# Kernel tuning notes

Hardware: AMD Instinct MI355X
Metric: run time of the kernel (lower is better)

Reference implementation:

```python
import jax, jax.numpy as jnp
from jax import lax
import numpy as np

L, B, C, H, W = 2, 4, 256, 128, 128
D = C // 2            # complex feature dim per head (embed_dim // 2)
NH = 2                # hardcoded n_heads in ComplexTransformerEncoderLayer
KS, STRIDE, PAD = 9, 8, 4
SCALE = 32.0 ** -0.5  # n_head_channels ** -0.5 (hardcoded 32)

_PNAMES = ['wq','bq','wk','bk','wv','bv','off_dw_w','off_dw_b','off_ln_g','off_ln_b',
           'off_pw_w','fc1_wr','fc1_wi','fc1_br','fc1_bi','fc2_wr','fc2_wi','fc2_br',
           'fc2_bi','ln_grr','ln_gri','ln_gii','ln_br','ln_bi','rpe_table']


def _bilinear(img, grid):
    # img: (Cc, Hi, Wi); grid: (..., 2) with (x, y) in [-1, 1]
    # matches F.grid_sample(mode='bilinear', align_corners=True, padding_mode='zeros')
    Cc, Hi, Wi = img.shape
    x = (grid[..., 0] + 1.0) * 0.5 * (Wi - 1)
    y = (grid[..., 1] + 1.0) * 0.5 * (Hi - 1)
    x0 = jnp.floor(x); y0 = jnp.floor(y)
    x1 = x0 + 1.0; y1 = y0 + 1.0
    wx1 = x - x0; wx0 = 1.0 - wx1
    wy1 = y - y0; wy0 = 1.0 - wy1

    def tap(yy, xx, wgt):
        valid = (xx >= 0) & (xx <= Wi - 1) & (yy >= 0) & (yy <= Hi - 1)
        xi = jnp.clip(xx, 0, Wi - 1).astype(jnp.int32)
        yi = jnp.clip(yy, 0, Hi - 1).astype(jnp.int32)
        v = img[:, yi, xi]                      # (Cc, *grid_shape)
        return v * (wgt * valid.astype(img.dtype))[None]

    return (tap(y0, x0, wy0 * wx0) + tap(y0, x1, wy0 * wx1)
            + tap(y1, x0, wy1 * wx0) + tap(y1, x1, wy1 * wx1))

_grid_sample = jax.vmap(_bilinear)


def _cln(a, b, gam, eps=1e-20):
    # complex layer-norm via 2x2 covariance whitening over the last (feature) dim
    grr, gri, gii, br, bi = gam
    a = a - a.mean(-1, keepdims=True)
    b = b - b.mean(-1, keepdims=True)
    vrr = (a * a).mean(-1, keepdims=True) + eps
    vii = (b * b).mean(-1, keepdims=True) + eps
    vri = (a * b).mean(-1, keepdims=True)
    s = jnp.sqrt(vrr * vii - vri * vri)
    t = jnp.sqrt(vrr + vii + 2.0 * s)
    inv = 1.0 / (s * t)
    wrr = (vii + s) * inv; wii = (vrr + s) * inv; wri = -vri * inv
    na = wrr * a + wri * b
    nb = wri * a + wii * b
    return grr * na + gri * nb + br, gri * na + gii * nb + bi


def _layer(xa, xb, p):
    res_a = xa.reshape(B * NH, D, H * W).transpose(2, 0, 1)  # (HW, B*NH, D)
    res_b = xb.reshape(B * NH, D, H * W).transpose(2, 0, 1)

    def proj(x, w, bias):  # 1x1 conv
        return jnp.einsum('bchw,oc->bohw', x, w) + bias[None, :, None, None]

    qa = proj(xa, p['wq'], p['bq'])
    qb = proj(xb, p['wq'], p['bq'])

    def conv_offset(q):
        y = lax.conv_general_dilated(q, p['off_dw_w'], (STRIDE, STRIDE),
                                     ((PAD, PAD), (PAD, PAD)),
                                     feature_group_count=C,
                                     dimension_numbers=('NCHW', 'OIHW', 'NCHW'))
        y = y + p['off_dw_b'][None, :, None, None]
        m = y.mean(1, keepdims=True)
        v = ((y - m) ** 2).mean(1, keepdims=True)
        y = (y - m) * lax.rsqrt(v + 1e-5)
        y = y * p['off_ln_g'][None, :, None, None] + p['off_ln_b'][None, :, None, None]
        y = jax.nn.gelu(y, approximate=False)
        return jnp.einsum('bchw,pc->bhwp', y, p['off_pw_w'])  # (B, Hk, Wk, 2) in (y, x)

    off_a = conv_offset(qa)
    off_b = conv_offset(qb)
    Hk, Wk = off_a.shape[1], off_a.shape[2]
    ns = Hk * Wk

    ry = jnp.linspace(0.5, Hk - 0.5, Hk) / (Hk - 1.0) * 2.0 - 1.0
    rx = jnp.linspace(0.5, Wk - 0.5, Wk) / (Wk - 1.0) * 2.0 - 1.0
    ref = jnp.stack(jnp.meshgrid(ry, rx, indexing='ij'), -1)  # (Hk, Wk, 2) (y, x)
    pos_a = off_a + ref
    pos_b = off_b + ref

    xs_a = _grid_sample(xa, pos_a[..., ::-1])  # (B, C, Hk, Wk)
    xs_b = _grid_sample(xb, pos_b[..., ::-1])

    ka = proj(xs_a, p['wk'], p['bk']).reshape(B * NH, D, ns)
    va = proj(xs_a, p['wv'], p['bv']).reshape(B * NH, D, ns)
    kb = proj(xs_b, p['wk'], p['bk']).reshape(B * NH, D, ns)
    vb = proj(xs_b, p['wv'], p['bv']).reshape(B * NH, D, ns)
    qa_ = qa.reshape(B * NH, D, H * W)
    qb_ = qb.reshape(B * NH, D, H * W)

    # Re( q * conj(k) ); imaginary part is discarded by attn.real in the original
    attn = SCALE * (jnp.einsum('bcm,bcn->bmn', qa_, ka)
                    + jnp.einsum('bcm,bcn->bmn', qb_, kb))

    # deformable RPE bias; only the real (a) branch survives attn.real
    gy = jnp.arange(H, dtype=xa.dtype) / (H - 1.0) * 2.0 - 1.0
    gx = jnp.arange(W, dtype=xa.dtype) / (W - 1.0) * 2.0 - 1.0
    qg = jnp.stack(jnp.meshgrid(gy, gx, indexing='ij'), -1).reshape(H * W, 2)
    disp_a = (qg[None, :, None, :] - pos_a.reshape(B, ns, 2)[:, None, :, :]) * 0.5
    rpe = jnp.broadcast_to(p['rpe_table'][None], (B, NH, 2 * H - 1, 2 * W - 1))
    bias_a = _grid_sample(rpe, disp_a[..., ::-1]).reshape(B * NH, H * W, ns)

    attn = jax.nn.softmax(attn + bias_a, axis=2)
    oa = jnp.einsum('bmn,bcn->bcm', attn, va).transpose(2, 0, 1)  # (HW, B*NH, D)
    ob = jnp.einsum('bmn,bcn->bcm', attn, vb).transpose(2, 0, 1)

    oa, ob = _cln(oa, ob, (p['ln_grr'][0], p['ln_gri'][0], p['ln_gii'][0],
                           p['ln_br'][0], p['ln_bi'][0]))
    xa2 = res_a + oa
    xb2 = res_b + ob

    def clinear(a, b, wr, wi, br, bi):
        ya = a @ wr.T - b @ wi.T + br
        yb = a @ wi.T + b @ wr.T + bi
        return ya, yb

    ha, hb = clinear(xa2, xb2, p['fc1_wr'], p['fc1_wi'], p['fc1_br'], p['fc1_bi'])
    ha = jax.nn.relu(ha); hb = jax.nn.relu(hb)
    ha, hb = clinear(ha, hb, p['fc2_wr'], p['fc2_wi'], p['fc2_br'], p['fc2_bi'])
    ha, hb = _cln(ha, hb, (p['ln_grr'][1], p['ln_gri'][1], p['ln_gii'][1],
                           p['ln_br'][1], p['ln_bi'][1]))
    xa3 = xa2 + ha
    xb3 = xb2 + hb
    return (xa3.transpose(1, 2, 0).reshape(B, C, H, W),
            xb3.transpose(1, 2, 0).reshape(B, C, H, W))


def _forward(x_A, x_B, stacked):
    for l in range(L):
        p = {n: stacked[n][l] for n in _PNAMES}
        x_A, x_B = _layer(x_A, x_B, p)
    return x_A, x_B


def setup_inputs():
    key = jax.random.key(0)
    ks = jax.random.split(key, 12)
    f32 = jnp.float32
    return {
        'x_A': jax.random.normal(ks[0], (B, C, H, W), f32),
        'x_B': jax.random.normal(ks[1], (B, C, H, W), f32),
        'wq': jax.random.normal(ks[2], (L, C, C), f32) / np.float32(np.sqrt(C)),
        'bq': jnp.zeros((L, C), f32),
        'wk': jax.random.normal(ks[3], (L, C, C), f32) / np.float32(np.sqrt(C)),
        'bk': jnp.zeros((L, C), f32),
        'wv': jax.random.normal(ks[4], (L, C, C), f32) / np.float32(np.sqrt(C)),
        'bv': jnp.zeros((L, C), f32),
        'off_dw_w': jax.random.normal(ks[5], (L, C, 1, KS, KS), f32) * 0.05,
        'off_dw_b': jnp.zeros((L, C), f32),
        'off_ln_g': jnp.ones((L, C), f32),
        'off_ln_b': jnp.zeros((L, C), f32),
        'off_pw_w': jax.random.normal(ks[6], (L, 2, C), f32) * 0.01,
        'fc1_wr': jax.random.normal(ks[7], (L, D, D), f32) / np.float32(np.sqrt(D)),
        'fc1_wi': jax.random.normal(ks[8], (L, D, D), f32) / np.float32(np.sqrt(D)),
        'fc1_br': jnp.zeros((L, D), f32),
        'fc1_bi': jnp.zeros((L, D), f32),
        'fc2_wr': jax.random.normal(ks[9], (L, D, D), f32) / np.float32(np.sqrt(D)),
        'fc2_wi': jax.random.normal(ks[10], (L, D, D), f32) / np.float32(np.sqrt(D)),
        'fc2_br': jnp.zeros((L, D), f32),
        'fc2_bi': jnp.zeros((L, D), f32),
        'ln_grr': jnp.full((L, 2, D), 1.0 / np.sqrt(2.0), f32),
        'ln_gri': jnp.zeros((L, 2, D), f32),
        'ln_gii': jnp.full((L, 2, D), 1.0 / np.sqrt(2.0), f32),
        'ln_br': jnp.zeros((L, 2, D), f32),
        'ln_bi': jnp.zeros((L, 2, D), f32),
        # original forward creates rpe_table as fresh zeros each call
        'rpe_table': jnp.zeros((L, NH, 2 * H - 1, 2 * W - 1), f32),
    }


def reference(x_A, x_B, wq, bq, wk, bk, wv, bv, off_dw_w, off_dw_b, off_ln_g, off_ln_b,
              off_pw_w, fc1_wr, fc1_wi, fc1_br, fc1_bi, fc2_wr, fc2_wi, fc2_br, fc2_bi,
              ln_grr, ln_gri, ln_gii, ln_br, ln_bi, rpe_table):
    vals = (wq, bq, wk, bk, wv, bv, off_dw_w, off_dw_b, off_ln_g, off_ln_b, off_pw_w,
            fc1_wr, fc1_wi, fc1_br, fc1_bi, fc2_wr, fc2_wi, fc2_br, fc2_bi,
            ln_grr, ln_gri, ln_gii, ln_br, ln_bi, rpe_table)
    stacked = {n: v for n, v in zip(_PNAMES, vals)}
    return _forward(x_A, x_B, stacked)
```

## Files before the change

### kernel.cpp

```cpp
#include <hip/hip_runtime.h>
#include <math.h>

#define DEVFN static __device__ __forceinline__

constexpr int LAYERS = 2;
constexpr int Bz = 4;
constexpr int Cc = 256;
constexpr int Hh = 128;
constexpr int Ww = 128;
constexpr int Dd = 128;
constexpr int NHh = 2;
constexpr int BHt = Bz * NHh;
constexpr int Mt  = Hh * Ww;
constexpr int HK = 16, WK = 16;
constexpr int NSs = HK * WK;
constexpr int STR = 8, PADc = 4;
constexpr int RPH = 2*Hh - 1, RPW = 2*Ww - 1;
constexpr float SCALE_F = 0.17677669529663687f;

typedef __attribute__((ext_vector_type(8))) short  bf16x8;
typedef __attribute__((ext_vector_type(4))) float  f32x4;

DEVFN float wsum64(float v) {
    #pragma unroll
    for (int off = 32; off > 0; off >>= 1) v += __shfl_xor(v, off, 64);
    return v;
}

DEVFN void split2(float x, ushort& h, ushort& l)
{
    const uint u  = __float_as_uint(x);
    const uint hb = (u + 0x7fffu + ((u >> 16) & 1u)) & 0xffff0000u;
    h = (ushort)(hb >> 16);
    const float r = x - __uint_as_float(hb);
    const uint ul = __float_as_uint(r);
    l = (ushort)((ul + 0x7fffu + ((ul >> 16) & 1u)) >> 16);
}

DEVFN ushort f2bf(float x)
{
    const uint u = __float_as_uint(x);
    return (ushort)((u + 0x7fffu + ((u >> 16) & 1u)) >> 16);
}
DEVFN float bf2f(ushort s) { return __uint_as_float(((uint)s) << 16); }

DEVFN uint shfu(uint v, int src) { return (uint)__shfl((int)v, src, 64); }

DEVFN bf16x8 pack4(uint a, uint b, uint c, uint d)
{
    union { uint u[4]; bf16x8 v; } t;
    t.u[0] = a; t.u[1] = b; t.u[2] = c; t.u[3] = d;
    return t.v;
}

DEVFN void unpack8(uint4 a, uint4 b, bf16x8& h, bf16x8& l)
{
    const uint u[8] = {a.x, a.y, a.z, a.w, b.x, b.y, b.z, b.w};
    #pragma unroll
    for (int j = 0; j < 8; j++) {
        h[j] = (short)(u[j] >> 16);
        l[j] = (short)(u[j] & 0xffffu);
    }
}

__global__ __launch_bounds__(256)
void k_proj(const float* __restrict__ X, const float* __restrict__ W,
            const float* __restrict__ bias, float* __restrict__ Out, int Mdim)
{
    __shared__ float wsm[16][64];
    __shared__ float xsm[16][64];
    const int tid = threadIdx.x;
    const int m0 = blockIdx.x * 64;
    const int o0 = blockIdx.y * 64;
    const float* Xb = X + (size_t)blockIdx.z * Cc * Mdim;
    float* Ob = Out + (size_t)blockIdx.z * Cc * Mdim;
    const int to = tid >> 4;
    const int tm = tid & 15;
    float acc[4][4] = {{0.f}};
    for (int k0 = 0; k0 < Cc; k0 += 16) {
        {
            const int i = tid >> 2, kq = tid & 3;
            float4 w4 = *(const float4*)(W + (size_t)(o0 + i)*Cc + k0 + kq*4);
            wsm[kq*4+0][i] = w4.x; wsm[kq*4+1][i] = w4.y;
            wsm[kq*4+2][i] = w4.z; wsm[kq*4+3][i] = w4.w;
            const int kk = tid >> 4, jq = tid & 15;
            *(float4*)&xsm[kk][jq*4] =
                *(const float4*)(Xb + (size_t)(k0 + kk)*Mdim + m0 + jq*4);
        }
        __syncthreads();
        #pragma unroll
        for (int kk = 0; kk < 16; kk++) {
            float4 a4 = *(const float4*)&wsm[kk][to*4];
            float4 b4 = *(const float4*)&xsm[kk][tm*4];
            float av[4] = {a4.x, a4.y, a4.z, a4.w};
            float bv[4] = {b4.x, b4.y, b4.z, b4.w};
            #pragma unroll
            for (int ii = 0; ii < 4; ii++)
                #pragma unroll
                for (int jj = 0; jj < 4; jj++)
                    acc[ii][jj] += av[ii] * bv[jj];
        }
        __syncthreads();
    }
    #pragma unroll
    for (int ii = 0; ii < 4; ii++) {
        const int o = o0 + to*4 + ii;
        const float bo = bias[o];
        float4 r4 = make_float4(acc[ii][0]+bo, acc[ii][1]+bo, acc[ii][2]+bo, acc[ii][3]+bo);
        *(float4*)(Ob + (size_t)o*Mdim + m0 + tm*4) = r4;
    }
}

__global__ __launch_bounds__(256)
void k_dwconv(const float* __restrict__ Q, const float* __restrict__ Wdw,
              const float* __restrict__ Bdw, float* __restrict__ Y)
{
    const int c = blockIdx.x, b = blockIdx.y;
    __shared__ float wsmem[81];
    const int tid = threadIdx.x;
    if (tid < 81) wsmem[tid] = Wdw[c*81 + tid];
    __syncthreads();
    const int i = tid >> 4, j = tid & 15;
    const float* Qc = Q + ((size_t)b*Cc + c)*Mt;
    float acc = Bdw[c];
    const int ybase = i*STR - PADc, xbase = j*STR - PADc;
    #pragma unroll
    for (int u = 0; u < 9; u++) {
        const int y = ybase + u;
        if (y < 0 || y >= Hh) continue;
        #pragma unroll
        for (int v = 0; v < 9; v++) {
            const int x = xbase + v;
            if (x < 0 || x >= Ww) continue;
            acc += wsmem[u*9+v] * Qc[y*Ww + x];
        }
    }
    Y[((size_t)b*Cc + c)*NSs + i*WK + j] = acc;
}

DEVFN float block_reduce(float v, float* red, int tid)
{
    red[tid] = v; __syncthreads();
    #pragma unroll
    for (int s2 = 128; s2 > 0; s2 >>= 1) {
        if (tid < s2) red[tid] += red[tid + s2];
        __syncthreads();
    }
    const float r = red[0];
    __syncthreads();
    return r;
}

__global__ __launch_bounds__(256)
void k_lnpw(const float* __restrict__ Y, const float* __restrict__ G,
            const float* __restrict__ Bt, const float* __restrict__ PW,
            float* __restrict__ Pos)
{
    __shared__ float red[256];
    const int ij = blockIdx.x, b = blockIdx.y;
    const int tid = threadIdx.x;
    const float y = Y[((size_t)b*Cc + tid)*NSs + ij];
    const float m = block_reduce(y, red, tid) * (1.f/256.f);
    const float d = y - m;
    const float v = block_reduce(d*d, red, tid) * (1.f/256.f);
    const float g = d * rsqrtf(v + 1e-5f) * G[tid] + Bt[tid];
    const float ge = 0.5f * g * (1.f + erff(g * 0.70710678118654752f));
    const float off0 = block_reduce(ge * PW[tid], red, tid);
    const float off1 = block_reduce(ge * PW[Cc + tid], red, tid);
    if (tid == 0) {
        const int i = ij >> 4, j = ij & 15;
        const float refy = ((float)i + 0.5f) * (2.f/15.f) - 1.f;
        const float refx = ((float)j + 0.5f) * (2.f/15.f) - 1.f;
        Pos[((size_t)b*NSs + ij)*2 + 0] = off0 + refy;
        Pos[((size_t)b*NSs + ij)*2 + 1] = off1 + refx;
    }
}

__global__ __launch_bounds__(256)
void k_gsample(const float* __restrict__ X, const float* __restrict__ Pos,
               float* __restrict__ Xs)
{
    const int c = blockIdx.x, b = blockIdx.y, s = threadIdx.x;
    const float py = Pos[((size_t)b*NSs + s)*2 + 0];
    const float px = Pos[((size_t)b*NSs + s)*2 + 1];
    const float x = (px + 1.f) * 0.5f * (float)(Ww - 1);
    const float y = (py + 1.f) * 0.5f * (float)(Hh - 1);
    const float x0 = floorf(x), y0 = floorf(y);
    const float wx1 = x - x0, wx0 = 1.f - wx1;
    const float wy1 = y - y0, wy0 = 1.f - wy1;
    const float* Xc = X + ((size_t)b*Cc + c)*Mt;
    float acc = 0.f;
    #pragma unroll
    for (int t = 0; t < 4; t++) {
        const float xx = x0 + (float)(t & 1);
        const float yy = y0 + (float)(t >> 1);
        float w = ((t & 1) ? wx1 : wx0) * ((t >> 1) ? wy1 : wy0);
        const bool valid = (xx >= 0.f) && (xx <= (float)(Ww-1)) &&
                           (yy >= 0.f) && (yy <= (float)(Hh-1));
        const int xi = (int)fminf(fmaxf(xx, 0.f), (float)(Ww-1));
        const int yi = (int)fminf(fmaxf(yy, 0.f), (float)(Hh-1));
        acc += (valid ? w : 0.f) * Xc[yi*Ww + xi];
    }
    Xs[((size_t)b*Cc + c)*NSs + s] = acc;
}

__global__ __launch_bounds__(256)
void k_qsplit(const float* __restrict__ Qa, const float* __restrict__ Qb,
              uint* __restrict__ Qs)
{
    __shared__ float tile[64][65];
    const int tid = threadIdx.x;
    const int m0 = blockIdx.x * 64;
    const int bh = blockIdx.y;
    const int b = bh >> 1, h = bh & 1;
    for (int ccblk = 0; ccblk < 4; ccblk++) {
        #pragma unroll
        for (int i = 0; i < 4; i++) {
            const int idx = i*256 + tid;
            const int ccl = idx >> 4, mq = idx & 15;
            const int cc2 = ccblk*64 + ccl;
            const float* src = (cc2 >> 7) ? Qb : Qa;
            *(float4*)&tile[ccl][mq*4] =
                *(const float4*)(src + ((size_t)b*Cc + h*Dd + (cc2 & 127))*Mt + m0 + mq*4);
        }
        __syncthreads();
        #pragma unroll
        for (int i = 0; i < 16; i++) {
            const int idx = i*256 + tid;
            const int ml = idx >> 6, ccl = idx & 63;
            ushort hi, lo; split2(tile[ccl][ml], hi, lo);
            Qs[((size_t)bh*Mt + m0 + ml)*256 + ccblk*64 + ccl] = ((uint)hi << 16) | lo;
        }
        __syncthreads();
    }
}

__global__ __launch_bounds__(256)
void k_ksplit(const float* __restrict__ Ka, const float* __restrict__ Kb,
              uint* __restrict__ Ktp)
{
    __shared__ float tile[64][65];
    const int tid = threadIdx.x;
    const int n0 = blockIdx.x * 64;
    const int bh = blockIdx.y;
    const int b = bh >> 1, h = bh & 1;
    for (int ccblk = 0; ccblk < 4; ccblk++) {
        #pragma unroll
        for (int i = 0; i < 16; i++) {
            const int idx = i*256 + tid;
            const int ccl = idx >> 6, nl = idx & 63;
            const int cc2 = ccblk*64 + ccl;
            const float* src = (cc2 >> 7) ? Kb : Ka;
            tile[ccl][nl] = src[((size_t)b*Cc + h*Dd + (cc2 & 127))*NSs + n0 + nl];
        }
        __syncthreads();
        #pragma unroll
        for (int i = 0; i < 16; i++) {
            const int idx = i*256 + tid;
            const int nl = idx >> 6, ccl = idx & 63;
            ushort hi, lo; split2(tile[ccl][nl], hi, lo);
            Ktp[((size_t)bh*NSs + n0 + nl)*256 + ccblk*64 + ccl] = ((uint)hi << 16) | lo;
        }
        __syncthreads();
    }
}

__global__ __launch_bounds__(256)
void k_vsplit(const float* __restrict__ Va, const float* __restrict__ Vb,
              uint* __restrict__ Vsp)
{
    const size_t e = (size_t)blockIdx.x*256 + threadIdx.x;
    const int n  = (int)(e & 255);
    const int j  = (int)((e >> 8) & 255);
    const int bh = (int)(e >> 16);
    const int b = bh >> 1, h = bh & 1;
    const float* src = (j >> 7) ? Vb : Va;
    const float v = src[((size_t)b*Cc + h*Dd + (j & 127))*NSs + n];
    ushort hi, lo; split2(v, hi, lo);
    Vsp[e] = ((uint)hi << 16) | lo;
}

__global__ __launch_bounds__(256)
void k_wsplit4(const float* __restrict__ W0, const float* __restrict__ W1,
               const float* __restrict__ W2, const float* __restrict__ W3,
               uint* __restrict__ Wp)
{
    const int mat = blockIdx.y;
    const float* W = (mat == 0) ? W0 : (mat == 1) ? W1 : (mat == 2) ? W2 : W3;
    const int i = blockIdx.x*256 + threadIdx.x;
    ushort hi, lo; split2(W[i], hi, lo);
    Wp[(size_t)mat*Dd*Dd + i] = ((uint)hi << 16) | lo;
}

__global__ __launch_bounds__(256, 2)
void k_attn_mfma(const uint* __restrict__ Qs, const uint* __restrict__ Ktp,
                 const uint* __restrict__ Vsp,
                 const float* __restrict__ Pos, const float* __restrict__ Rpe,
                 float* __restrict__ Oa, float* __restrict__ Ob)
{
    constexpr int GS = 66;
    __shared__ ushort Gt[NSs * GS];
    __shared__ float fxs[NSs];
    __shared__ __align__(16) uint kvbuf[2][4096];
    const int tid = threadIdx.x;
    const int m0 = blockIdx.x * 64;
    const int bh = blockIdx.y;
    const int b = bh >> 1, h = bh & 1;
    const int j0 = m0 & 127;
    const int iq = m0 >> 7;
    const float* Rh = Rpe + (size_t)h * RPH * RPW;

    {
        const int n = tid;
        const float py = Pos[((size_t)b*NSs + n)*2 + 0];
        const float px = Pos[((size_t)b*NSs + n)*2 + 1];
        const float xf = (float)j0 + 63.5f - 63.5f*px;
        const float yf = (float)iq + 63.5f - 63.5f*py;
        const float xbf = floorf(xf), ybf = floorf(yf);
        const float fx = xf - xbf, fy = yf - ybf;
        fxs[n] = fx;
        const int yb = (int)ybf;
        const float wy0 = (1.f - fy) * ((yb   >= 0 && yb   <= RPH-1) ? 1.f : 0.f);
        const float wy1 = fy         * ((yb+1 >= 0 && yb+1 <= RPH-1) ? 1.f : 0.f);
        const int y0c = yb   < 0 ? 0 : (yb   > RPH-1 ? RPH-1 : yb);
        const int y1c = yb+1 < 0 ? 0 : (yb+1 > RPH-1 ? RPH-1 : yb+1);
        const float* r0 = Rh + (size_t)y0c * RPW;
        const float* r1 = Rh + (size_t)y1c * RPW;
        const int xb = (int)xbf;
        #pragma unroll 4
        for (int t = 0; t <= 64; t++) {
            const int xi = xb + t;
            const int xc = xi < 0 ? 0 : (xi > RPW-1 ? RPW-1 : xi);
            const float v = wy0*r0[xc] + wy1*r1[xc];
            Gt[n*GS + t] = f2bf((xi >= 0 && xi <= RPW-1) ? v : 0.f);
        }
    }

    const int w = tid >> 6, l = tid & 63;
    const int l15 = l & 15, g = l >> 4;
    const int mcol = m0 + w*16 + l15;

    const uint* kbase = Ktp + (size_t)bh * 65536;
    const uint* vbase = Vsp + (size_t)bh * 65536;
    char* const kv0 = (char*)&kvbuf[0][0];
    char* const kv1 = (char*)&kvbuf[1][0];
    auto stage = [&](int p, const uint* chunk) {
        char* dst = p ? kv1 : kv0;
        #pragma unroll
        for (int r = 0; r < 4; r++) {
            const int idx = r*1024 + tid*4;
            const uint4 v = *(const uint4*)(chunk + idx);
            const int byte = idx << 2;
            const int swz = ((byte >> 10) & 7) << 4;
            *(uint4*)(dst + (byte ^ swz)) = v;
        }
    };

    bf16x8 qh[8], ql[8];
    {
        const uint* qp = Qs + ((size_t)bh*Mt + mcol)*256 + g*8;
        #pragma unroll
        for (int cs = 0; cs < 8; cs++) {
            const uint4 q0 = *(const uint4*)(qp + cs*32);
            const uint4 q1 = *(const uint4*)(qp + cs*32 + 4);
            unpack8(q0, q1, qh[cs], ql[cs]);
        }
    }

    f32x4 acc[16];
    #pragma unroll
    for (int nt = 0; nt < 16; nt++) acc[nt] = (f32x4){0.f, 0.f, 0.f, 0.f};

    const int rowb = l15 << 10;
    const int sw = (l15 & 7) << 4;

    stage(0, kbase);
    __syncthreads();
    #pragma unroll
    for (int nt = 0; nt < 16; nt++) {
        if (nt < 15) stage((nt + 1) & 1, kbase + (nt + 1)*4096);
        const char* bufc = (nt & 1) ? kv1 : kv0;
        #pragma unroll
        for (int cs = 0; cs < 8; cs++) {
            const int a0 = rowb + cs*128 + g*32;
            const uint4 k0 = *(const uint4*)(bufc + (a0 ^ sw));
            const uint4 k1 = *(const uint4*)(bufc + ((a0 + 16) ^ sw));
            bf16x8 kh, kl; unpack8(k0, k1, kh, kl);
            acc[nt] = __builtin_amdgcn_mfma_f32_16x16x32_bf16(kh, qh[cs], acc[nt], 0, 0, 0);
            acc[nt] = __builtin_amdgcn_mfma_f32_16x16x32_bf16(kh, ql[cs], acc[nt], 0, 0, 0);
            acc[nt] = __builtin_amdgcn_mfma_f32_16x16x32_bf16(kl, qh[cs], acc[nt], 0, 0, 0);
        }
        __syncthreads();
    }

    const int dm = w*16 + l15;
    float mx = -1e30f;
    #pragma unroll
    for (int nt = 0; nt < 16; nt++) {
        #pragma unroll
        for (int r = 0; r < 4; r++) {
            const int n = nt*16 + g*4 + r;
            const float g0 = bf2f(Gt[n*GS + dm]);
            const float g1 = bf2f(Gt[n*GS + dm + 1]);
            const float bias = g0 + fxs[n]*(g1 - g0);
            const float s = SCALE_F*acc[nt][r] + bias;
            acc[nt][r] = s;
            mx = fmaxf(mx, s);
        }
    }
    mx = fmaxf(mx, __shfl_xor(mx, 16, 64));
    mx = fmaxf(mx, __shfl_xor(mx, 32, 64));
    float sum = 0.f;
    #pragma unroll
    for (int nt = 0; nt < 16; nt++)
        #pragma unroll
        for (int r = 0; r < 4; r++) {
            const float e = __expf(acc[nt][r] - mx);
            acc[nt][r] = e;
            sum += e;
        }
    sum += __shfl_xor(sum, 16, 64);
    sum += __shfl_xor(sum, 32, 64);
    const float inv = 1.f / sum;

    uint hU0[16], hU1[16], lU0[16], lU1[16];
    #pragma unroll
    for (int nt = 0; nt < 16; nt++) {
        ushort ph_[4], pl_[4];
        #pragma unroll
        for (int r = 0; r < 4; r++) split2(acc[nt][r] * inv, ph_[r], pl_[r]);
        hU0[nt] = (uint)ph_[0] | ((uint)ph_[1] << 16);
        hU1[nt] = (uint)ph_[2] | ((uint)ph_[3] << 16);
        lU0[nt] = (uint)pl_[0] | ((uint)pl_[1] << 16);
        lU1[nt] = (uint)pl_[2] | ((uint)pl_[3] << 16);
    }

    const int srcA = (((2*g)     & 3) << 4) | l15;
    const int srcB = (((2*g + 1) & 3) << 4) | l15;
    const bool hi2 = (g >> 1) & 1;
    bf16x8 ph[8], pl[8];
    #pragma unroll
    for (int cs = 0; cs < 8; cs++) {
        uint A00 = shfu(hU0[2*cs], srcA), A01 = shfu(hU0[2*cs+1], srcA);
        uint A10 = shfu(hU1[2*cs], srcA), A11 = shfu(hU1[2*cs+1], srcA);
        uint B00 = shfu(hU0[2*cs], srcB), B01 = shfu(hU0[2*cs+1], srcB);
        uint B10 = shfu(hU1[2*cs], srcB), B11 = shfu(hU1[2*cs+1], srcB);
        ph[cs] = pack4(hi2 ? A01 : A00, hi2 ? A11 : A10,
                       hi2 ? B01 : B00, hi2 ? B11 : B10);
        A00 = shfu(lU0[2*cs], srcA); A01 = shfu(lU0[2*cs+1], srcA);
        A10 = shfu(lU1[2*cs], srcA); A11 = shfu(lU1[2*cs+1], srcA);
        B00 = shfu(lU0[2*cs], srcB); B01 = shfu(lU0[2*cs+1], srcB);
        B10 = shfu(lU1[2*cs], srcB); B11 = shfu(lU1[2*cs+1], srcB);
        pl[cs] = pack4(hi2 ? A01 : A00, hi2 ? A11 : A10,
                       hi2 ? B01 : B00, hi2 ? B11 : B10);
    }

    const size_t rowbase = ((size_t)bh*Mt + mcol)*Dd;
    stage(0, vbase);
    __syncthreads();
    for (int jt = 0; jt < 16; jt++) {
        if (jt < 15) stage((jt + 1) & 1, vbase + (jt + 1)*4096);
        const char* bufc = (jt & 1) ? kv1 : kv0;
        f32x4 a2 = (f32x4){0.f, 0.f, 0.f, 0.f};
        #pragma unroll
        for (int cs = 0; cs < 8; cs++) {
            const int a0 = rowb + cs*128 + g*32;
            const uint4 v0 = *(const uint4*)(bufc + (a0 ^ sw));
            const uint4 v1 = *(const uint4*)(bufc + ((a0 + 16) ^ sw));
            bf16x8 vh, vl; unpack8(v0, v1, vh, vl);
            a2 = __builtin_amdgcn_mfma_f32_16x16x32_bf16(vh, ph[cs], a2, 0, 0, 0);
            a2 = __builtin_amdgcn_mfma_f32_16x16x32_bf16(vh, pl[cs], a2, 0, 0, 0);
            a2 = __builtin_amdgcn_mfma_f32_16x16x32_bf16(vl, ph[cs], a2, 0, 0, 0);
        }
        const float4 o = make_float4(a2[0], a2[1], a2[2], a2[3]);
        const int jv0 = jt*16 + g*4;
        if (jt < 8) *(float4*)(Oa + rowbase + jv0) = o;
        else        *(float4*)(Ob + rowbase + jv0 - 128) = o;
        __syncthreads();
    }
}

__global__ __launch_bounds__(256)
void k_cln_attn(const float* __restrict__ Oa, const float* __restrict__ Ob,
                const float* __restrict__ Xa, const float* __restrict__ Xb,
                const float* __restrict__ Pgrr, const float* __restrict__ Pgri,
                const float* __restrict__ Pgii, const float* __restrict__ Pbr,
                const float* __restrict__ Pbi,
                float* __restrict__ X2a, float* __restrict__ X2b)
{
    __shared__ float ra[32][132];
    __shared__ float rb[32][132];
    const int tid = threadIdx.x;
    const int m0 = blockIdx.x * 32;
    const int bh = blockIdx.y;
    const int b = bh >> 1, h = bh & 1;
    {
        const float* Xpa = Xa + ((size_t)b*Cc + h*Dd)*Mt + m0;
        const float* Xpb = Xb + ((size_t)b*Cc + h*Dd)*Mt + m0;
        for (int idx = tid; idx < 1024; idx += 256) {
            const int c = idx >> 3, jq = idx & 7;
            float4 a4 = *(const float4*)(Xpa + (size_t)c*Mt + jq*4);
            float4 b4 = *(const float4*)(Xpb + (size_t)c*Mt + jq*4);
            ra[jq*4+0][c] = a4.x; ra[jq*4+1][c] = a4.y;
            ra[jq*4+2][c] = a4.z; ra[jq*4+3][c] = a4.w;
            rb[jq*4+0][c] = b4.x; rb[jq*4+1][c] = b4.y;
            rb[jq*4+2][c] = b4.z; rb[jq*4+3][c] = b4.w;
        }
    }
    __syncthreads();
    const int wave = tid >> 6, lane = tid & 63;
    const float grr0 = Pgrr[lane], grr1 = Pgrr[lane+64];
    const float gri0 = Pgri[lane], gri1 = Pgri[lane+64];
    const float gii0 = Pgii[lane], gii1 = Pgii[lane+64];
    const float br0  = Pbr[lane],  br1  = Pbr[lane+64];
    const float bi0  = Pbi[lane],  bi1  = Pbi[lane+64];
    for (int r = wave; r < 32; r += 4) {
        const size_t rowoff = ((size_t)bh*Mt + m0 + r)*Dd;
        float a0 = Oa[rowoff + lane], a1 = Oa[rowoff + lane + 64];
        float c0 = Ob[rowoff + lane], c1 = Ob[rowoff + lane + 64];
        const float ma = wsum64(a0 + a1) * (1.f/128.f);
        const float mb = wsum64(c0 + c1) * (1.f/128.f);
        a0 -= ma; a1 -= ma; c0 -= mb; c1 -= mb;
        const float vrr = wsum64(a0*a0 + a1*a1) * (1.f/128.f) + 1e-20f;
        const float vii = wsum64(c0*c0 + c1*c1) * (1.f/128.f) + 1e-20f;
        const float vri = wsum64(a0*c0 + a1*c1) * (1.f/128.f);
        const float s = sqrtf(fmaxf(vrr*vii - vri*vri, 0.f));
        const float t = sqrtf(vrr + vii + 2.f*s);
        const float inv = 1.f / (s*t);
        const float wrr = (vii + s)*inv, wii = (vrr + s)*inv, wri = -vri*inv;
        const float na0 = wrr*a0 + wri*c0, nb0 = wri*a0 + wii*c0;
        const float na1 = wrr*a1 + wri*c1, nb1 = wri*a1 + wii*c1;
        X2a[rowoff + lane]      = ra[r][lane]    + grr0*na0 + gri0*nb0 + br0;
        X2a[rowoff + lane + 64] = ra[r][lane+64] + grr1*na1 + gri1*nb1 + br1;
        X2b[rowoff + lane]      = rb[r][lane]    + gri0*na0 + gii0*nb0 + bi0;
        X2b[rowoff + lane + 64] = rb[r][lane+64] + gri1*na1 + gii1*nb1 + bi1;
    }
}

__global__ __launch_bounds__(256)
void k_ffn_mfma(const float* __restrict__ A, const float* __restrict__ Bm,
                const uint* __restrict__ Wrp, const uint* __restrict__ Wip,
                const float* __restrict__ br, const float* __restrict__ bi,
                float* __restrict__ Ha, float* __restrict__ Hb, int relu)
{
    const int tid = threadIdx.x;
    const size_t r0 = (size_t)blockIdx.x * 64;
    const int w = tid >> 6, l = tid & 63;
    const int l15 = l & 15, g = l >> 4;
    const size_t row = r0 + (size_t)w*16 + l15;

    f32x4 accr[8], acci[8];
    #pragma unroll
    for (int nt = 0; nt < 8; nt++) {
        accr[nt] = (f32x4){0.f, 0.f, 0.f, 0.f};
        acci[nt] = (f32x4){0.f, 0.f, 0.f, 0.f};
    }

    const float* ap = A  + row*Dd + g*8;
    const float* bp = Bm + row*Dd + g*8;
    const uint*  wr = Wrp + l15*Dd + g*8;
    const uint*  wi = Wip + l15*Dd + g*8;

    #pragma unroll
    for (int cs = 0; cs < 4; cs++) {
        const float4 a0 = *(const float4*)(ap + cs*32);
        const float4 a1 = *(const float4*)(ap + cs*32 + 4);
        const float4 b0 = *(const float4*)(bp + cs*32);
        const float4 b1 = *(const float4*)(bp + cs*32 + 4);
        const float av[8] = {a0.x,a0.y,a0.z,a0.w,a1.x,a1.y,a1.z,a1.w};
        const float bv[8] = {b0.x,b0.y,b0.z,b0.w,b1.x,b1.y,b1.z,b1.w};
        bf16x8 ah, al, bh_, bl_, nh, nl;
        #pragma unroll
        for (int j = 0; j < 8; j++) {
            ushort h1, l1; split2(av[j], h1, l1);
            ah[j] = (short)h1; al[j] = (short)l1;
            split2(bv[j], h1, l1);
            bh_[j] = (short)h1; bl_[j] = (short)l1;
            nh[j] = (short)(h1 ^ 0x8000);
            nl[j] = (short)(l1 ^ 0x8000);
        }
        #pragma unroll
        for (int nt = 0; nt < 8; nt++) {
            const uint* wrp2 = wr + nt*2048 + cs*32;
            const uint* wip2 = wi + nt*2048 + cs*32;
            const uint4 r0v = *(const uint4*)(wrp2);
            const uint4 r1v = *(const uint4*)(wrp2 + 4);
            const uint4 i0v = *(const uint4*)(wip2);
            const uint4 i1v = *(const uint4*)(wip2 + 4);
            bf16x8 wrh, wrl, wih, wil;
            unpack8(r0v, r1v, wrh, wrl);
            unpack8(i0v, i1v, wih, wil);
            accr[nt] = __builtin_amdgcn_mfma_f32_16x16x32_bf16(wrh, ah, accr[nt], 0, 0, 0);
            accr[nt] = __builtin_amdgcn_mfma_f32_16x16x32_bf16(wrh, al, accr[nt], 0, 0, 0);
            accr[nt] = __builtin_amdgcn_mfma_f32_16x16x32_bf16(wrl, ah, accr[nt], 0, 0, 0);
            accr[nt] = __builtin_amdgcn_mfma_f32_16x16x32_bf16(wih, nh, accr[nt], 0, 0, 0);
            accr[nt] = __builtin_amdgcn_mfma_f32_16x16x32_bf16(wih, nl, accr[nt], 0, 0, 0);
            accr[nt] = __builtin_amdgcn_mfma_f32_16x16x32_bf16(wil, nh, accr[nt], 0, 0, 0);
            acci[nt] = __builtin_amdgcn_mfma_f32_16x16x32_bf16(wih, ah, acci[nt], 0, 0, 0);
            acci[nt] = __builtin_amdgcn_mfma_f32_16x16x32_bf16(wih, al, acci[nt], 0, 0, 0);
            acci[nt] = __builtin_amdgcn_mfma_f32_16x16x32_bf16(wil, ah, acci[nt], 0, 0, 0);
            acci[nt] = __builtin_amdgcn_mfma_f32_16x16x32_bf16(wrh, bh_, acci[nt], 0, 0, 0);
            acci[nt] = __builtin_amdgcn_mfma_f32_16x16x32_bf16(wrh, bl_, acci[nt], 0, 0, 0);
            acci[nt] = __builtin_amdgcn_mfma_f32_16x16x32_bf16(wrl, bh_, acci[nt], 0, 0, 0);
        }
    }

    #pragma unroll
    for (int nt = 0; nt < 8; nt++) {
        const int n0 = nt*16 + g*4;
        const float4 vbr = *(const float4*)(br + n0);
        const float4 vbi = *(const float4*)(bi + n0);
        const float brv[4] = {vbr.x, vbr.y, vbr.z, vbr.w};
        const float biv[4] = {vbi.x, vbi.y, vbi.z, vbi.w};
        float4 orv, oiv;
        float* po = &orv.x; float* pj = &oiv.x;
        #pragma unroll
        for (int r = 0; r < 4; r++) {
            float hr = accr[nt][r] + brv[r];
            float hi = acci[nt][r] + biv[r];
            if (relu) { hr = fmaxf(hr, 0.f); hi = fmaxf(hi, 0.f); }
            po[r] = hr; pj[r] = hi;
        }
        *(float4*)(Ha + row*Dd + n0) = orv;
        *(float4*)(Hb + row*Dd + n0) = oiv;
    }
}

__global__ __launch_bounds__(256)
void k_cln_ffn(const float* __restrict__ Ha2, const float* __restrict__ Hb2,
               const float* __restrict__ X2a, const float* __restrict__ X2b,
               const float* __restrict__ Pgrr, const float* __restrict__ Pgri,
               const float* __restrict__ Pgii, const float* __restrict__ Pbr,
               const float* __restrict__ Pbi,
               float* __restrict__ OutA, float* __restrict__ OutB)
{
    __shared__ float oA[128][36];
    __shared__ float oB[128][36];
    const int tid = threadIdx.x;
    const int m0 = blockIdx.x * 32;
    const int bh = blockIdx.y;
    const int b = bh >> 1, h = bh & 1;
    const int wave = tid >> 6, lane = tid & 63;
    const float grr0 = Pgrr[lane], grr1 = Pgrr[lane+64];
    const float gri0 = Pgri[lane], gri1 = Pgri[lane+64];
    const float gii0 = Pgii[lane], gii1 = Pgii[lane+64];
    const float br0  = Pbr[lane],  br1  = Pbr[lane+64];
    const float bi0  = Pbi[lane],  bi1  = Pbi[lane+64];
    for (int r = wave; r < 32; r += 4) {
        const size_t rowoff = ((size_t)bh*Mt + m0 + r)*Dd;
        float a0 = Ha2[rowoff + lane], a1 = Ha2[rowoff + lane + 64];
        float c0 = Hb2[rowoff + lane], c1 = Hb2[rowoff + lane + 64];
        const float ma = wsum64(a0 + a1) * (1.f/128.f);
        const float mb = wsum64(c0 + c1) * (1.f/128.f);
        a0 -= ma; a1 -= ma; c0 -= mb; c1 -= mb;
        const float vrr = wsum64(a0*a0 + a1*a1) * (1.f/128.f) + 1e-20f;
        const float vii = wsum64(c0*c0 + c1*c1) * (1.f/128.f) + 1e-20f;
        const float vri = wsum64(a0*c0 + a1*c1) * (1.f/128.f);
        const float s = sqrtf(fmaxf(vrr*vii - vri*vri, 0.f));
        const float t = sqrtf(vrr + vii + 2.f*s);
        const float inv = 1.f / (s*t);
        const float wrr = (vii + s)*inv, wii = (vrr + s)*inv, wri = -vri*inv;
        const float na0 = wrr*a0 + wri*c0, nb0 = wri*a0 + wii*c0;
        const float na1 = wrr*a1 + wri*c1, nb1 = wri*a1 + wii*c1;
        oA[lane][r]    = X2a[rowoff + lane]      + grr0*na0 + gri0*nb0 + br0;
        oA[lane+64][r] = X2a[rowoff + lane + 64] + grr1*na1 + gri1*nb1 + br1;
        oB[lane][r]    = X2b[rowoff + lane]      + gri0*na0 + gii0*nb0 + bi0;
        oB[lane+64][r] = X2b[rowoff + lane + 64] + gri1*na1 + gii1*nb1 + bi1;
    }
    __syncthreads();
    const size_t obase = ((size_t)b*Cc + h*Dd)*Mt + m0;
    for (int idx = tid; idx < 1024; idx += 256) {
        const int c = idx >> 3, jq = idx & 7;
        *(float4*)(OutA + obase + (size_t)c*Mt + jq*4) = *(const float4*)&oA[c][jq*4];
        *(float4*)(OutB + obase + (size_t)c*Mt + jq*4) = *(const float4*)&oB[c][jq*4];
    }
}

extern "C" void kernel_launch(void* const* d_in, const int* in_sizes, int n_in,
                              void* d_out, int out_size, void* d_ws, size_t ws_size,
                              hipStream_t stream)
{
    const float* xA0 = (const float*)d_in[0];
    const float* xB0 = (const float*)d_in[1];
    const float* wq  = (const float*)d_in[2];
    const float* bq  = (const float*)d_in[3];
    const float* wk  = (const float*)d_in[4];
    const float* bk  = (const float*)d_in[5];
    const float* wv  = (const float*)d_in[6];
    const float* bv  = (const float*)d_in[7];
    const float* dww = (const float*)d_in[8];
    const float* dwb = (const float*)d_in[9];
    const float* lng = (const float*)d_in[10];
    const float* lnb = (const float*)d_in[11];
    const float* pw  = (const float*)d_in[12];
    const float* f1wr = (const float*)d_in[13];
    const float* f1wi = (const float*)d_in[14];
    const float* f1br = (const float*)d_in[15];
    const float* f1bi = (const float*)d_in[16];
    const float* f2wr = (const float*)d_in[17];
    const float* f2wi = (const float*)d_in[18];
    const float* f2br = (const float*)d_in[19];
    const float* f2bi = (const float*)d_in[20];
    const float* lgrr = (const float*)d_in[21];
    const float* lgri = (const float*)d_in[22];
    const float* lgii = (const float*)d_in[23];
    const float* lbr  = (const float*)d_in[24];
    const float* lbi  = (const float*)d_in[25];
    const float* rpe  = (const float*)d_in[26];

    float* ws = (float*)d_ws;
    const size_t NB = (size_t)Bz * Cc * Mt;
    const size_t SC = (size_t)Bz * Cc * NSs;
    float* Pa  = ws;        float* Pb  = Pa  + NB;
    float* Ra  = Pb  + NB;  float* Rb  = Ra  + NB;
    float* Ya  = Rb  + NB;  float* Yb  = Ya  + SC;
    float* XsA = Yb  + SC;  float* XsB = XsA + SC;
    float* Kab = XsB + SC;  float* Kbb = Kab + SC;
    float* Vab = Kbb + SC;  float* Vbb = Vab + SC;
    float* Sp0 = Vbb + SC;  float* Sp1 = Sp0 + SC;
    float* PosA = Sp1 + SC; float* PosB = PosA + (size_t)Bz*NSs*2;
    float* Wpf  = PosB + (size_t)Bz*NSs*2;

    uint* Qs  = (uint*)Ra;
    uint* Ktp = (uint*)Sp0;
    uint* Vsp = (uint*)Ya;
    uint* Wp  = (uint*)Wpf;

    float* outAf = (float*)d_out;
    float* outBf = outAf + NB;

    for (int l = 0; l < LAYERS; l++) {
        const float* pwq = wq + (size_t)l*Cc*Cc;
        const float* pbq = bq + (size_t)l*Cc;
        const float* pwk = wk + (size_t)l*Cc*Cc;
        const float* pbk = bk + (size_t)l*Cc;
        const float* pwv = wv + (size_t)l*Cc*Cc;
        const float* pbv = bv + (size_t)l*Cc;
        const float* pdww = dww + (size_t)l*Cc*81;
        const float* pdwb = dwb + (size_t)l*Cc;
        const float* plng = lng + (size_t)l*Cc;
        const float* plnb = lnb + (size_t)l*Cc;
        const float* ppw  = pw  + (size_t)l*2*Cc;
        const float* p1wr = f1wr + (size_t)l*Dd*Dd;
        const float* p1wi = f1wi + (size_t)l*Dd*Dd;
        const float* p1br = f1br + (size_t)l*Dd;
        const float* p1bi = f1bi + (size_t)l*Dd;
        const float* p2wr = f2wr + (size_t)l*Dd*Dd;
        const float* p2wi = f2wi + (size_t)l*Dd*Dd;
        const float* p2br = f2br + (size_t)l*Dd;
        const float* p2bi = f2bi + (size_t)l*Dd;
        const float* g0rr = lgrr + (size_t)(l*2+0)*Dd;
        const float* g0ri = lgri + (size_t)(l*2+0)*Dd;
        const float* g0ii = lgii + (size_t)(l*2+0)*Dd;
        const float* g0br = lbr  + (size_t)(l*2+0)*Dd;
        const float* g0bi = lbi  + (size_t)(l*2+0)*Dd;
        const float* g1rr = lgrr + (size_t)(l*2+1)*Dd;
        const float* g1ri = lgri + (size_t)(l*2+1)*Dd;
        const float* g1ii = lgii + (size_t)(l*2+1)*Dd;
        const float* g1br = lbr  + (size_t)(l*2+1)*Dd;
        const float* g1bi = lbi  + (size_t)(l*2+1)*Dd;
        const float* prpe = rpe + (size_t)l*NHh*RPH*RPW;

        const float* inA = l ? outAf : xA0;
        const float* inB = l ? outBf : xB0;

        dim3 gW(64, 4);
        k_wsplit4<<<gW, 256, 0, stream>>>(p1wr, p1wi, p2wr, p2wi, Wp);

        dim3 gP(Mt/64, Cc/64, Bz);
        k_proj<<<gP, 256, 0, stream>>>(inA, pwq, pbq, Pa, Mt);
        k_proj<<<gP, 256, 0, stream>>>(inB, pwq, pbq, Pb, Mt);

        dim3 gD(Cc, Bz);
        k_dwconv<<<gD, 256, 0, stream>>>(Pa, pdww, pdwb, Ya);
        k_dwconv<<<gD, 256, 0, stream>>>(Pb, pdww, pdwb, Yb);

        dim3 gL(NSs, Bz);
        k_lnpw<<<gL, 256, 0, stream>>>(Ya, plng, plnb, ppw, PosA);
        k_lnpw<<<gL, 256, 0, stream>>>(Yb, plng, plnb, ppw, PosB);

        dim3 gS(Cc, Bz);
        k_gsample<<<gS, 256, 0, stream>>>(inA, PosA, XsA);
        k_gsample<<<gS, 256, 0, stream>>>(inB, PosB, XsB);

        dim3 gKV(NSs/64, Cc/64, Bz);
        k_proj<<<gKV, 256, 0, stream>>>(XsA, pwk, pbk, Kab, NSs);
        k_proj<<<gKV, 256, 0, stream>>>(XsB, pwk, pbk, Kbb, NSs);
        k_proj<<<gKV, 256, 0, stream>>>(XsA, pwv, pbv, Vab, NSs);
        k_proj<<<gKV, 256, 0, stream>>>(XsB, pwv, pbv, Vbb, NSs);

        dim3 gKs(NSs/64, BHt);
        k_ksplit<<<gKs, 256, 0, stream>>>(Kab, Kbb, Ktp);
        k_vsplit<<<2048, 256, 0, stream>>>(Vab, Vbb, Vsp);
        dim3 gQs(Mt/64, BHt);
        k_qsplit<<<gQs, 256, 0, stream>>>(Pa, Pb, Qs);

        dim3 gA(Mt/64, BHt);
        k_attn_mfma<<<gA, 256, 0, stream>>>(Qs, Ktp, Vsp, PosA, prpe, Pa, Pb);

        dim3 gC(Mt/32, BHt);
        k_cln_attn<<<gC, 256, 0, stream>>>(Pa, Pb, inA, inB,
                                           g0rr, g0ri, g0ii, g0br, g0bi, Ra, Rb);

        dim3 gF((unsigned)((size_t)BHt*Mt/64));
        k_ffn_mfma<<<gF, 256, 0, stream>>>(Ra, Rb, Wp, Wp + (size_t)Dd*Dd,
                                           p1br, p1bi, Pa, Pb, 1);
        k_ffn_mfma<<<gF, 256, 0, stream>>>(Pa, Pb, Wp + (size_t)2*Dd*Dd,
                                           Wp + (size_t)3*Dd*Dd,
                                           p2br, p2bi, Pa, Pb, 0);

        k_cln_ffn<<<gC, 256, 0, stream>>>(Pa, Pb, Ra, Rb,
                                          g1rr, g1ri, g1ii, g1br, g1bi, outAf, outBf);
    }
    (void)in_sizes; (void)n_in; (void)out_size; (void)ws_size;
}
```

Before: 2.679 ms.

## Compute Q projection with split-bf16 MFMA instead of scalar FP32 GEMM

Replaces the FP32 SIMT Q-projection GEMM with an MFMA kernel. It reuses the qsplit kernel to split the input activations into bf16 hi/lo pairs in a transposed layout, and a new kernel splits the Q weight the same way. Three bf16 MFMAs per tile emulate near-FP32 precision, and the result goes through shared memory to keep the channel-major output layout. This adds extra split passes and workspace traffic, and the hi/lo emulation drops the lo*lo term, which slightly reduces accuracy.

```diff
diff --git a/kernel.cpp b/kernel.cpp
--- a/kernel.cpp
+++ b/kernel.cpp
@@ -112,6 +112,69 @@
 }
 
 __global__ __launch_bounds__(256)
+void k_projq_mfma(const uint* __restrict__ Xt, const uint* __restrict__ Wqp,
+                  const float* __restrict__ bias, float* __restrict__ Out,
+                  int s)
+{
+    __shared__ __align__(16) float ot[256 * 68];
+    const int tid = threadIdx.x;
+    const int m0 = blockIdx.x * 64;
+    const int b  = blockIdx.y;
+    const int w = tid >> 6, l = tid & 63;
+    const int l15 = l & 15, g = l >> 4;
+    const int m = m0 + w*16 + l15;
+
+    bf16x8 xh[8], xl[8];
+    {
+        const uint* xp0 = Xt + ((size_t)(b*2 + 0)*Mt + m)*256 + s*128 + g*8;
+        const uint* xp1 = Xt + ((size_t)(b*2 + 1)*Mt + m)*256 + s*128 + g*8;
+        #pragma unroll
+        for (int cs = 0; cs < 8; cs++) {
+            const uint* xp = ((cs < 4) ? xp0 : xp1) + (cs & 3)*32;
+            const uint4 x0 = *(const uint4*)(xp);
+            const uint4 x1 = *(const uint4*)(xp + 4);
+            unpack8(x0, x1, xh[cs], xl[cs]);
+        }
+    }
+
+    f32x4 acc[16];
+    #pragma unroll
+    for (int nt = 0; nt < 16; nt++) acc[nt] = (f32x4){0.f, 0.f, 0.f, 0.f};
+
+    const uint* wp = Wqp + l15*256 + g*8;
+    #pragma unroll
+    for (int cs = 0; cs < 8; cs++) {
+        #pragma unroll
+        for (int nt = 0; nt < 16; nt++) {
+            const uint* wpp = wp + nt*4096 + cs*32;
+            const uint4 w0 = *(const uint4*)(wpp);
+            const uint4 w1 = *(const uint4*)(wpp + 4);
+            bf16x8 wh, wl; unpack8(w0, w1, wh, wl);
+            acc[nt] = __builtin_amdgcn_mfma_f32_16x16x32_bf16(wh, xh[cs], acc[nt], 0, 0, 0);
+            acc[nt] = __builtin_amdgcn_mfma_f32_16x16x32_bf16(wh, xl[cs], acc[nt], 0, 0, 0);
+            acc[nt] = __builtin_amdgcn_mfma_f32_16x16x32_bf16(wl, xh[cs], acc[nt], 0, 0, 0);
+        }
+    }
+
+    #pragma unroll
+    for (int nt = 0; nt < 16; nt++) {
+        #pragma unroll
+        for (int r = 0; r < 4; r++) {
+            const int o = nt*16 + g*4 + r;
+            ot[o*68 + w*16 + l15] = acc[nt][r] + bias[o];
+        }
+    }
+    __syncthreads();
+    #pragma unroll
+    for (int it = 0; it < 16; it++) {
+        const int idx = it*256 + tid;
+        const int o = idx >> 4, mq = idx & 15;
+        const float4 v = *(const float4*)&ot[o*68 + mq*4];
+        *(float4*)(Out + ((size_t)b*Cc + o)*Mt + m0 + mq*4) = v;
+    }
+}
+
+__global__ __launch_bounds__(256)
 void k_dwconv(const float* __restrict__ Q, const float* __restrict__ Wdw,
               const float* __restrict__ Bdw, float* __restrict__ Y)
 {
@@ -290,6 +353,14 @@
     const int i = blockIdx.x*256 + threadIdx.x;
     ushort hi, lo; split2(W[i], hi, lo);
     Wp[(size_t)mat*Dd*Dd + i] = ((uint)hi << 16) | lo;
+}
+
+__global__ __launch_bounds__(256)
+void k_wsplit1(const float* __restrict__ W, uint* __restrict__ Wp)
+{
+    const int i = blockIdx.x*256 + threadIdx.x;
+    ushort hi, lo; split2(W[i], hi, lo);
+    Wp[i] = ((uint)hi << 16) | lo;
 }
 
 __global__ __launch_bounds__(256, 2)
@@ -725,6 +796,7 @@
     uint* Ktp = (uint*)Sp0;
     uint* Vsp = (uint*)Ya;
     uint* Wp  = (uint*)Wpf;
+    uint* Wqp = Wp + (size_t)4*Dd*Dd;
 
     float* outAf = (float*)d_out;
     float* outBf = outAf + NB;
@@ -766,10 +838,14 @@
 
         dim3 gW(64, 4);
         k_wsplit4<<<gW, 256, 0, stream>>>(p1wr, p1wi, p2wr, p2wi, Wp);
-
-        dim3 gP(Mt/64, Cc/64, Bz);
-        k_proj<<<gP, 256, 0, stream>>>(inA, pwq, pbq, Pa, Mt);
-        k_proj<<<gP, 256, 0, stream>>>(inB, pwq, pbq, Pb, Mt);
+        k_wsplit1<<<256, 256, 0, stream>>>(pwq, Wqp);
+
+        dim3 gQs(Mt/64, BHt);
+        k_qsplit<<<gQs, 256, 0, stream>>>(inA, inB, Qs);
+
+        dim3 gPQ(Mt/64, Bz);
+        k_projq_mfma<<<gPQ, 256, 0, stream>>>(Qs, Wqp, pbq, Pa, 0);
+        k_projq_mfma<<<gPQ, 256, 0, stream>>>(Qs, Wqp, pbq, Pb, 1);
 
         dim3 gD(Cc, Bz);
         k_dwconv<<<gD, 256, 0, stream>>>(Pa, pdww, pdwb, Ya);
@@ -792,7 +868,6 @@
         dim3 gKs(NSs/64, BHt);
         k_ksplit<<<gKs, 256, 0, stream>>>(Kab, Kbb, Ktp);
         k_vsplit<<<2048, 256, 0, stream>>>(Vab, Vbb, Vsp);
-        dim3 gQs(Mt/64, BHt);
         k_qsplit<<<gQs, 256, 0, stream>>>(Pa, Pb, Qs);
 
         dim3 gA(Mt/64, BHt);
```

Result: slower. 2.864 ms (+6.9%).
